# Optimization experiments

Measured on AMD Instinct MI355X. Metric: run time of the kernel, lower is better.

## Reference

```python
import jax, jax.numpy as jnp
import numpy as np

B = 8
A = 3
LEVEL_HW = [(200, 304), (100, 152), (50, 76), (25, 38), (13, 19)]
LEVEL_SIZES = [A * h * w for h, w in LEVEL_HW]  # anchors per level
N_TOTAL = sum(LEVEL_SIZES)                      # 242991
IMG_H, IMG_W = 800.0, 1216.0
PRE_NMS_TOP_N = 2000
POST_NMS_TOP_N = 100
NMS_THRESH = 0.7
MIN_SIZE = 1e-3
BBOX_XFORM_CLIP = float(np.log(1000.0 / 16.0))
NEG = -1e30


def setup_inputs() -> dict:
    key = jax.random.key(0)
    ks = jax.random.split(key, 2 * len(LEVEL_HW) + 3)
    inp = {}
    for i, (h, w) in enumerate(LEVEL_HW):
        inp[f"cls{i}"] = jax.random.normal(ks[2 * i], (B, A, h, w), dtype=jnp.float32)
        inp[f"box{i}"] = jax.random.normal(ks[2 * i + 1], (B, 4 * A, h, w), dtype=jnp.float32) * 0.5
    kc, kw, _ = ks[-3], ks[-2], ks[-1]
    c = jax.random.uniform(kc, (N_TOTAL, 2), dtype=jnp.float32) * jnp.array([IMG_W, IMG_H], jnp.float32)
    wh = 16.0 + jax.random.uniform(kw, (N_TOTAL, 2), dtype=jnp.float32) * 240.0
    inp["anchors"] = jnp.concatenate([c - 0.5 * wh, c + 0.5 * wh], axis=-1)  # x1y1x2y2
    return inp


def _permute_flatten(p, C):
    # [N, A*C, H, W] -> [N, H*W*A, C]  (matches permute_and_flatten)
    n, ac, h, w = p.shape
    a = ac // C
    return p.reshape(n, a, C, h, w).transpose(0, 3, 4, 1, 2).reshape(n, -1, C)


def _decode(deltas, anchors):
    wa = anchors[:, 2] - anchors[:, 0]
    ha = anchors[:, 3] - anchors[:, 1]
    cxa = anchors[:, 0] + 0.5 * wa
    cya = anchors[:, 1] + 0.5 * ha
    dx, dy = deltas[..., 0], deltas[..., 1]
    dw = jnp.minimum(deltas[..., 2], BBOX_XFORM_CLIP)
    dh = jnp.minimum(deltas[..., 3], BBOX_XFORM_CLIP)
    cx = dx * wa + cxa
    cy = dy * ha + cya
    pw = jnp.exp(dw) * wa
    ph = jnp.exp(dh) * ha
    return jnp.stack([cx - 0.5 * pw, cy - 0.5 * ph, cx + 0.5 * pw, cy + 0.5 * ph], axis=-1)


def _nms_single(boxes, scores, lvl, valid):
    # batched_nms: offset boxes by level so cross-level boxes never overlap
    off = lvl.astype(boxes.dtype)[:, None] * (max(IMG_H, IMG_W) + 1.0)
    b0 = boxes + off
    s0 = jnp.where(valid, scores, NEG)  # small-box removal -> impossible to pick
    order = jnp.argsort(-s0)
    b = b0[order]
    s = s0[order]
    areas = (b[:, 2] - b[:, 0]) * (b[:, 3] - b[:, 1])
    suppressed0 = s <= NEG / 2
    idx_range = jnp.arange(s.shape[0])

    def step(suppressed, _):
        avail = jnp.where(suppressed, NEG, s)
        i = jnp.argmax(avail)
        ok = avail[i] > NEG / 2
        bi = b[i]
        xx1 = jnp.maximum(b[:, 0], bi[0])
        yy1 = jnp.maximum(b[:, 1], bi[1])
        xx2 = jnp.minimum(b[:, 2], bi[2])
        yy2 = jnp.minimum(b[:, 3], bi[3])
        inter = jnp.maximum(xx2 - xx1, 0.0) * jnp.maximum(yy2 - yy1, 0.0)
        union = areas + areas[i] - inter
        iou = jnp.where(union > 0, inter / union, 0.0)
        sup_new = suppressed | (iou > NMS_THRESH) | (idx_range == i)
        return jnp.where(ok, sup_new, suppressed), (jnp.where(ok, order[i], 0), ok)

    _, (sel, selv) = jax.lax.scan(step, suppressed0, None, length=POST_NMS_TOP_N)
    out_boxes = jnp.where(selv[:, None], boxes[sel], 0.0)
    out_scores = jnp.where(selv, scores[sel], 0.0)
    return out_boxes, out_scores


def reference(cls0, cls1, cls2, cls3, cls4, box0, box1, box2, box3, box4, anchors):
    cls_levels = [cls0, cls1, cls2, cls3, cls4]
    box_levels = [box0, box1, box2, box3, box4]
    pred_class = jnp.concatenate([_permute_flatten(c, 1) for c in cls_levels], axis=1)  # [B,N,1]
    deltas = jnp.concatenate([_permute_flatten(b, 4) for b in box_levels], axis=1)      # [B,N,4]
    proposals = _decode(deltas, anchors)                                               # [B,N,4]
    scores = pred_class[..., 0]                                                        # [B,N]

    # per-level top-k; replicates the original's cumulative k = min(k, num_anchor)
    keep, lvl = [], []
    k, off = PRE_NMS_TOP_N, 0
    for li, n in enumerate(LEVEL_SIZES):
        k = min(k, n)
        _, idx = jax.lax.top_k(scores[:, off:off + n], k)
        keep.append(idx + off)
        lvl.append(jnp.full((k,), li, dtype=jnp.int32))
        off += n
    keep = jnp.concatenate(keep, axis=1)   # [B,K]
    lvl = jnp.concatenate(lvl)             # [K]

    prop = jnp.take_along_axis(proposals, keep[..., None], axis=1)  # [B,K,4]
    sc = jnp.take_along_axis(scores, keep, axis=1)                  # [B,K]
    prop = jnp.stack([
        jnp.clip(prop[..., 0], 0.0, IMG_W), jnp.clip(prop[..., 1], 0.0, IMG_H),
        jnp.clip(prop[..., 2], 0.0, IMG_W), jnp.clip(prop[..., 3], 0.0, IMG_H)], axis=-1)
    valid = ((prop[..., 2] - prop[..., 0]) >= MIN_SIZE) & ((prop[..., 3] - prop[..., 1]) >= MIN_SIZE)
    boxes_out, scores_out = jax.vmap(lambda bx, s, v: _nms_single(bx, s, lvl, v))(prop, sc, valid)
    return boxes_out, scores_out  # [B,100,4], [B,100]
```

## Files before the change

### kernel.cpp

```cpp
#include <hip/hip_runtime.h>
#include <cstdint>

#define NTOT 242991
#define BATCH 8
#define KTOT 8741
#define CAP 8192
#define NBIN 4096
#define CSTR 16
#define MEMTOT 1943928
#define SLICE 256
#define RSTR 9
#define BCAP 2048
#define NB2 2048
#define DBLK 9

__device__ __forceinline__ int level_of(int n) {
    if (n < 182400) return 0;
    if (n < 228000) return 1;
    if (n < 239400) return 2;
    if (n < 242250) return 3;
    return 4;
}

__device__ __forceinline__ void locate(int n, int& l, int& H, int& W, int& loc) {
    if (n < 182400)      { l = 0; H = 200; W = 304; loc = n; }
    else if (n < 228000) { l = 1; H = 100; W = 152; loc = n - 182400; }
    else if (n < 239400) { l = 2; H = 50;  W = 76;  loc = n - 228000; }
    else if (n < 242250) { l = 3; H = 25;  W = 38;  loc = n - 239400; }
    else                 { l = 4; H = 13;  W = 19;  loc = n - 242250; }
}

__device__ __forceinline__ int classify_bl(int x) {
    int l, HW;
    if (x < 1459200)      { l = 0; HW = 60800; }
    else if (x < 1824000) { l = 1; HW = 15200; x -= 1459200; }
    else if (x < 1915200) { l = 2; HW = 3800;  x -= 1824000; }
    else if (x < 1938000) { l = 3; HW = 950;   x -= 1915200; }
    else                  { l = 4; HW = 247;   x -= 1938000; }
    return (x / (3 * HW)) * 5 + l;
}

__device__ __forceinline__ void mem_decompose(int x, int& b, int& n, int& bl) {
    int HW, off, l;
    if (x < 1459200)      { l = 0; HW = 60800; off = 0; }
    else if (x < 1824000) { l = 1; HW = 15200; off = 182400; x -= 1459200; }
    else if (x < 1915200) { l = 2; HW = 3800;  off = 228000; x -= 1824000; }
    else if (x < 1938000) { l = 3; HW = 950;   off = 239400; x -= 1915200; }
    else                  { l = 4; HW = 247;   off = 242250; x -= 1938000; }
    int seg = 3 * HW;
    b = x / seg; int r = x - b * seg;
    int a = r / HW, pix = r - a * HW;
    n = off + pix * 3 + a;
    bl = b * 5 + l;
}

__device__ __forceinline__ float read_cls(int gid, const float* c0, const float* c1,
                                          const float* c2, const float* c3, const float* c4) {
    return (gid < 1459200) ? c0[gid] :
           (gid < 1824000) ? c1[gid - 1459200] :
           (gid < 1915200) ? c2[gid - 1824000] :
           (gid < 1938000) ? c3[gid - 1915200] : c4[gid - 1938000];
}

__device__ __forceinline__ uint32_t suffix_scan_1024(uint32_t g, uint32_t* lds16, int t) {
    int lane = t & 63, wid = t >> 6;
    uint32_t v = g;
#pragma unroll
    for (int o = 1; o < 64; o <<= 1) {
        uint32_t oth = __shfl_down(v, o, 64);
        if (lane + o < 64) v += oth;
    }
    if (lane == 0) lds16[wid] = v;
    __syncthreads();
    uint32_t w = 0;
    for (int q = wid + 1; q < 16; q++) w += lds16[q];
    __syncthreads();
    return v + w;
}

__device__ __forceinline__ uint32_t prefix_scan_1024(uint32_t g, uint32_t* lds16, int t) {
    int lane = t & 63, wid = t >> 6;
    uint32_t v = g;
#pragma unroll
    for (int o = 1; o < 64; o <<= 1) {
        uint32_t oth = __shfl_up(v, o, 64);
        if (lane >= o) v += oth;
    }
    if (lane == 63) lds16[wid] = v;
    __syncthreads();
    uint32_t w = 0;
    for (int q = 0; q < wid; q++) w += lds16[q];
    __syncthreads();
    return v + w;
}

__device__ __forceinline__ bool iou_hit(float bx1, float by1, float bx2, float by2, float ca,
                                        float4 sv) {
    float xx1 = fmaxf(bx1, sv.x), yy1 = fmaxf(by1, sv.y);
    float xx2 = fminf(bx2, sv.z), yy2 = fminf(by2, sv.w);
    float inter = fmaxf(xx2 - xx1, 0.f) * fmaxf(yy2 - yy1, 0.f);
    float sa = (sv.z - sv.x) * (sv.w - sv.y);
    float un = ca + sa - inter;
    return (un > 0.f) && (inter / un > 0.7f);
}

__global__ __launch_bounds__(1024)
void k_keys(const float* __restrict__ c0, const float* __restrict__ c1,
            const float* __restrict__ c2, const float* __restrict__ c3,
            const float* __restrict__ c4, uint32_t* __restrict__ hist) {
    int t = threadIdx.x;
    int base = blockIdx.x * 1024;
    int gid = base + t;
    bool in = gid < MEMTOT;
    __shared__ uint32_t lh[NBIN];

    int bl = 0, b, n;
    uint32_t u = 0;
    if (in) {
        mem_decompose(gid, b, n, bl);
        float sv = read_cls(gid, c0, c1, c2, c3, c4);
        u = __float_as_uint(sv);
        u ^= (u >> 31) ? 0xFFFFFFFFu : 0x80000000u;
    }
    int blf = classify_bl(base);
    int bll = classify_bl(min(base + 1023, MEMTOT - 1));
    if (blf == bll) {
        for (int j = t; j < NBIN; j += 1024) lh[j] = 0u;
        __syncthreads();
        if (in) atomicAdd(&lh[u >> 20], 1u);
        __syncthreads();
        uint32_t* gh = hist + (size_t)blf * NBIN;
        for (int j = t; j < NBIN; j += 1024) {
            uint32_t v = lh[j];
            if (v) atomicAdd(&gh[j], v);
        }
    } else {
        if (in) atomicAdd(&hist[(size_t)bl * NBIN + (u >> 20)], 1u);
    }
}

__global__ void k_bins(const uint32_t* __restrict__ hist, int* __restrict__ binT,
                       int* __restrict__ rrem) {
    int bl = blockIdx.x;
    const uint32_t* h = hist + (size_t)bl * NBIN;
    int l = bl % 5;
    uint32_t k = (l == 4) ? 741u : 2000u;
    __shared__ uint32_t ts[256];
    __shared__ uint32_t sb[256];
    int t = threadIdx.x;
    uint32_t hh[16];
#pragma unroll
    for (int i = 0; i < 16; i++) hh[i] = h[t * 16 + i];
    uint32_t s = 0;
#pragma unroll
    for (int i = 0; i < 16; i++) s += hh[i];
    ts[t] = s; sb[t] = s;
    __syncthreads();
    for (int d = 1; d < 256; d <<= 1) {
        uint32_t add = (t + d < 256) ? sb[t + d] : 0u;
        __syncthreads();
        sb[t] += add;
        __syncthreads();
    }
    uint32_t inc = sb[t], excl = inc - ts[t];
    if (excl < k && inc >= k) {
        uint32_t cum = excl;
#pragma unroll
        for (int i = 15; i >= 0; i--) {
            if (cum + hh[i] >= k) { binT[bl] = t * 16 + i; rrem[bl] = (int)(k - cum); break; }
            cum += hh[i];
        }
    }
}

__global__ __launch_bounds__(1024)
void k_compact(const float* __restrict__ c0, const float* __restrict__ c1,
               const float* __restrict__ c2, const float* __restrict__ c3,
               const float* __restrict__ c4, const int* __restrict__ binT,
               uint32_t* __restrict__ keep_n, uint32_t* __restrict__ keep_u,
               uint32_t* __restrict__ keep_cnt,
               uint32_t* __restrict__ cand_n, uint32_t* __restrict__ cand_u,
               uint32_t* __restrict__ cand_cnt) {
    int gid = blockIdx.x * 1024 + threadIdx.x;
    bool in = gid < MEMTOT;
    int b = 0, n = 0, bl = 0;
    uint32_t u = 0;
    if (in) {
        mem_decompose(gid, b, n, bl);
        float sv = read_cls(gid, c0, c1, c2, c3, c4);
        u = __float_as_uint(sv);
        u ^= (u >> 31) ? 0xFFFFFFFFu : 0x80000000u;
    }
    int T = in ? binT[bl] : 0x7FFFFFFF;
    int bin = (int)(u >> 20);
    bool pk = in && (bin > T);
    bool pc = in && (bin == T);
    int lane = threadIdx.x & 63;

    unsigned long long act = __ballot(in);
    if (act == 0ull) return;
    int lead = __ffsll(act) - 1;
    int bl0 = __shfl(bl, lead, 64);
    bool unif = (__ballot(in && (bl == bl0)) == act);
    if (unif) {
        int b0 = bl0 / 5, l0 = bl0 % 5;
        uint32_t kbase = (uint32_t)(b0 * KTOT + l0 * 2000);
        unsigned long long mk = __ballot(pk);
        if (mk) {
            int leader = __ffsll(mk) - 1;
            uint32_t bs = 0;
            if (lane == leader) bs = atomicAdd(&keep_cnt[bl0 * CSTR], (uint32_t)__popcll(mk));
            bs = __shfl(bs, leader, 64);
            if (pk) {
                uint32_t p = kbase + bs + (uint32_t)__popcll(mk & ((1ull << lane) - 1ull));
                keep_n[p] = (uint32_t)n; keep_u[p] = u;
            }
        }
        unsigned long long mc = __ballot(pc);
        if (mc) {
            int leader = __ffsll(mc) - 1;
            uint32_t bs = 0;
            if (lane == leader) bs = atomicAdd(&cand_cnt[bl0 * CSTR], (uint32_t)__popcll(mc));
            bs = __shfl(bs, leader, 64);
            if (pc) {
                uint32_t p = bs + (uint32_t)__popcll(mc & ((1ull << lane) - 1ull));
                if (p < CAP) {
                    cand_n[(size_t)bl0 * CAP + p] = (uint32_t)n;
                    cand_u[(size_t)bl0 * CAP + p] = u;
                }
            }
        }
    } else {
        int b1 = bl / 5, l1 = bl % 5;
        if (pk) {
            uint32_t p = atomicAdd(&keep_cnt[bl * CSTR], 1u);
            uint32_t q = (uint32_t)(b1 * KTOT + l1 * 2000) + p;
            keep_n[q] = (uint32_t)n; keep_u[q] = u;
        }
        if (pc) {
            uint32_t p = atomicAdd(&cand_cnt[bl * CSTR], 1u);
            if (p < CAP) {
                cand_n[(size_t)bl * CAP + p] = (uint32_t)n;
                cand_u[(size_t)bl * CAP + p] = u;
            }
        }
    }
}

__global__ __launch_bounds__(1024)
void k_select(const uint32_t* __restrict__ cand_n, const uint32_t* __restrict__ cand_u,
              const uint32_t* __restrict__ cand_cnt, const int* __restrict__ rrem,
              uint32_t* __restrict__ keep_n, uint32_t* __restrict__ keep_u,
              uint32_t* __restrict__ keep_cnt) {
    int bl = blockIdx.x;
    int b = bl / 5, l = bl % 5;
    int C = (int)min(cand_cnt[bl * CSTR], (uint32_t)CAP);
    int r = rrem[bl];
    const uint32_t* cdn = cand_n + (size_t)bl * CAP;
    const uint32_t* cdu = cand_u + (size_t)bl * CAP;
    __shared__ uint32_t hist_l[2048];
    __shared__ uint32_t lds16[16];
    __shared__ unsigned long long pref_sh;
    __shared__ uint32_t kk_sh;
    int t = threadIdx.x;
    if (t == 0) { pref_sh = 0ull; kk_sh = (uint32_t)r; }
    unsigned long long maskAcc = 0ull;
    const int shifts[5] = {41, 30, 19, 8, 0};
    const uint32_t masks[5] = {0x7FFu, 0x7FFu, 0x7FFu, 0x7FFu, 0xFFu};
    __syncthreads();
    for (int p = 0; p < 5; p++) {
        int shift = shifts[p];
        uint32_t msk = masks[p];
        for (int j = t; j < 2048; j += 1024) hist_l[j] = 0u;
        __syncthreads();
        unsigned long long pref = pref_sh;
        uint32_t kk = kk_sh;
        for (int i = t; i < C; i += 1024) {
            unsigned long long key =
                ((unsigned long long)cdu[i] << 32) | (uint32_t)(~cdn[i]);
            if ((key & maskAcc) == pref)
                atomicAdd(&hist_l[(uint32_t)(key >> shift) & msk], 1u);
        }
        __syncthreads();
        uint32_t g = hist_l[2 * t] + hist_l[2 * t + 1];
        uint32_t inc = suffix_scan_1024(g, lds16, t);
        uint32_t excl = inc - g;
        if (excl < kk && inc >= kk) {
            uint32_t hh1 = hist_l[2 * t + 1];
            uint32_t digit, rem;
            if (excl + hh1 >= kk) { digit = 2 * t + 1; rem = kk - excl; }
            else { digit = 2 * t; rem = kk - (excl + hh1); }
            pref_sh = pref | ((unsigned long long)digit << shift);
            kk_sh = rem;
        }
        __syncthreads();
        maskAcc |= (unsigned long long)msk << shift;
    }
    unsigned long long Tk = pref_sh;
    __syncthreads();
    int lane = t & 63;
    for (int i0 = 0; i0 < C; i0 += 1024) {
        int i = i0 + t;
        bool in = i < C;
        uint32_t n = in ? cdn[i] : 0u;
        uint32_t u = in ? cdu[i] : 0u;
        unsigned long long key = in ?
            (((unsigned long long)u << 32) | (uint32_t)(~n)) : 0ull;
        bool pr = in && ((key & maskAcc) >= Tk);
        unsigned long long mk = __ballot(pr);
        if (mk) {
            int leader = __ffsll(mk) - 1;
            uint32_t bs = 0;
            if (lane == leader) bs = atomicAdd(&keep_cnt[bl * CSTR], (uint32_t)__popcll(mk));
            bs = __shfl(bs, leader, 64);
            if (pr) {
                uint32_t p = (uint32_t)(b * KTOT + l * 2000) + bs +
                             (uint32_t)__popcll(mk & ((1ull << lane) - 1ull));
                keep_n[p] = n; keep_u[p] = u;
            }
        }
    }
}

__global__ __launch_bounds__(1024)
void k_decode(const float* __restrict__ b0, const float* __restrict__ b1,
              const float* __restrict__ b2, const float* __restrict__ b3,
              const float* __restrict__ b4, const float* __restrict__ anchors,
              const uint32_t* __restrict__ keep_n, const uint32_t* __restrict__ keep_u,
              float4* __restrict__ nbox, unsigned long long* __restrict__ nkey,
              uint32_t* __restrict__ shist) {
    int blk = blockIdx.x;
    int b = blk / DBLK, seg = blk % DBLK;
    int i = seg * 1024 + threadIdx.x;
    int t = threadIdx.x;
    __shared__ uint32_t lh[NBIN];
    for (int j = t; j < NBIN; j += 1024) lh[j] = 0u;
    __syncthreads();
    if (i < KTOT) {
        int gid = b * KTOT + i;
        int n = (int)keep_n[gid];
        uint32_t u = keep_u[gid];
        int l, H, W, loc; locate(n, l, H, W, loc);
        int a = loc % 3, hw = loc / 3;
        int w = hw % W, h = hw / W;
        const float* bp = (l == 0) ? b0 : (l == 1) ? b1 : (l == 2) ? b2 : (l == 3) ? b3 : b4;
        int HW = H * W;
        int base = ((b * 12 + a * 4) * H + h) * W + w;
        float dx = bp[base], dy = bp[base + HW];
        float dw = bp[base + 2 * HW], dh = bp[base + 3 * HW];
        float ax1 = anchors[4 * n], ay1 = anchors[4 * n + 1];
        float ax2 = anchors[4 * n + 2], ay2 = anchors[4 * n + 3];
        float wa = ax2 - ax1, ha = ay2 - ay1;
        float cxa = ax1 + 0.5f * wa, cya = ay1 + 0.5f * ha;
        const float CLIPV = 4.135166556742356f;
        dw = fminf(dw, CLIPV); dh = fminf(dh, CLIPV);
        float cx = dx * wa + cxa, cy = dy * ha + cya;
        float pw = expf(dw) * wa, ph = expf(dh) * ha;
        float x1 = cx - 0.5f * pw, y1 = cy - 0.5f * ph;
        float x2 = cx + 0.5f * pw, y2 = cy + 0.5f * ph;
        x1 = fminf(fmaxf(x1, 0.f), 1216.f); x2 = fminf(fmaxf(x2, 0.f), 1216.f);
        y1 = fminf(fmaxf(y1, 0.f), 800.f);  y2 = fminf(fmaxf(y2, 0.f), 800.f);
        bool valid = ((x2 - x1) >= 1e-3f) && ((y2 - y1) >= 1e-3f);
        float off = (float)l * 1217.0f;
        nbox[gid] = make_float4(x1 + off, y1 + off, x2 + off, y2 + off);
        nkey[gid] = valid ? (((unsigned long long)u << 32) | (uint32_t)(~n)) : 0ull;
        if (valid) atomicAdd(&lh[u >> 20], 1u);
    }
    __syncthreads();
    uint32_t* gh = shist + (size_t)b * NBIN;
    for (int j = t; j < NBIN; j += 1024) {
        uint32_t v = lh[j];
        if (v) atomicAdd(&gh[j], v);
    }
}

__global__ __launch_bounds__(1024)
void k_nms(const unsigned long long* __restrict__ nkey, const float4* __restrict__ nbox,
           const uint32_t* __restrict__ shist,
           unsigned long long* __restrict__ skey, float4* __restrict__ sbox,
           float* __restrict__ out) {
    int b = blockIdx.x, t = threadIdx.x, lane = t & 63, wid = t >> 6;
    unsigned long long* SK = skey + (size_t)b * KTOT;
    float4* BXs = sbox + (size_t)b * KTOT;

    __shared__ unsigned short bstart16[NBIN];
    __shared__ unsigned short bcnt16[NBIN];
    __shared__ unsigned long long k_l[BCAP];
    __shared__ unsigned short p_l[BCAP];
    __shared__ uint32_t scratch[4096];
    __shared__ float4 sel_l[100];
    __shared__ uint32_t sup[SLICE / 32];
    __shared__ uint32_t lds16[16];
    __shared__ uint32_t V_sh, picks_sh, bend_sh, fat_sh;
    __shared__ unsigned long long gmax_sh;
    __shared__ uint32_t jpos_sh;
    __shared__ unsigned long long wred[16];

    const uint32_t* H = shist + (size_t)b * NBIN;
    uint32_t h0 = H[4 * t], h1 = H[4 * t + 1], h2 = H[4 * t + 2], h3 = H[4 * t + 3];
    uint32_t g = h0 + h1 + h2 + h3;
    uint32_t inc = suffix_scan_1024(g, lds16, t);
    if (t == 0) { V_sh = inc; picks_sh = 0u; }
    uint32_t acc = inc - g;
    uint32_t* scur32 = scratch;
    bstart16[4 * t + 3] = (unsigned short)acc; bcnt16[4 * t + 3] = (unsigned short)h3;
    scur32[4 * t + 3] = acc; acc += h3;
    bstart16[4 * t + 2] = (unsigned short)acc; bcnt16[4 * t + 2] = (unsigned short)h2;
    scur32[4 * t + 2] = acc; acc += h2;
    bstart16[4 * t + 1] = (unsigned short)acc; bcnt16[4 * t + 1] = (unsigned short)h1;
    scur32[4 * t + 1] = acc; acc += h1;
    bstart16[4 * t + 0] = (unsigned short)acc; bcnt16[4 * t + 0] = (unsigned short)h0;
    scur32[4 * t + 0] = acc;
    __syncthreads();

#pragma unroll
    for (int e = 0; e < DBLK; e++) {
        int i = t + e * 1024;
        if (i < KTOT) {
            unsigned long long kk = nkey[(size_t)b * KTOT + i];
            if (kk != 0ull) {
                uint32_t q = (uint32_t)(kk >> 52);
                uint32_t p = atomicAdd(&scur32[q], 1u);
                SK[p] = kk;
                BXs[p] = nbox[(size_t)b * KTOT + i];
            }
        }
    }
    __threadfence();
    __syncthreads();

    uint32_t V = V_sh;
    uint32_t picks = 0;
    uint32_t P = 0;
    while (P < V && picks < 100u) {
        uint32_t target = min(P + (uint32_t)BCAP, V);
        if (t == 0) { bend_sh = P; fat_sh = P; }
        __syncthreads();
        for (int q = t; q < NBIN; q += 1024) {
            uint32_t c = bcnt16[q];
            if (c) {
                uint32_t s = bstart16[q];
                if (s >= P && s + c <= target) atomicMax(&bend_sh, s + c);
                if (s == P) fat_sh = P + c;
            }
        }
        __syncthreads();
        uint32_t B = bend_sh;

        if (B > P) {
            uint32_t total = B - P;
            uint32_t* hist2 = scratch;
            uint32_t* scur2 = scratch + 2048;
            for (int j = t; j < NB2; j += 1024) hist2[j] = 0u;
            __syncthreads();
            unsigned long long k0 = 0ull, k1 = 0ull;
            uint32_t bin0 = 0xFFFFFFFFu, bin1 = 0xFFFFFFFFu;
            uint32_t j0 = P + (uint32_t)t, j1 = P + (uint32_t)t + 1024u;
            if (j0 < B) {
                k0 = SK[j0];
                uint32_t q = (uint32_t)(k0 >> 52);
                uint32_t c = bcnt16[q], rel = (uint32_t)bstart16[q] - P;
                uint32_t sub = (uint32_t)((k0 >> 44) & 0xFFull);
                bin0 = rel + ((c * (255u - sub)) >> 8);
                atomicAdd(&hist2[bin0], 1u);
            }
            if (j1 < B) {
                k1 = SK[j1];
                uint32_t q = (uint32_t)(k1 >> 52);
                uint32_t c = bcnt16[q], rel = (uint32_t)bstart16[q] - P;
                uint32_t sub = (uint32_t)((k1 >> 44) & 0xFFull);
                bin1 = rel + ((c * (255u - sub)) >> 8);
                atomicAdd(&hist2[bin1], 1u);
            }
            __syncthreads();
            uint32_t g0 = hist2[2 * t], g1 = hist2[2 * t + 1];
            uint32_t incp = prefix_scan_1024(g0 + g1, lds16, t);
            uint32_t excl = incp - (g0 + g1);
            scur2[2 * t] = excl; scur2[2 * t + 1] = excl + g0;
            __syncthreads();
            if (bin0 != 0xFFFFFFFFu) {
                uint32_t pos = atomicAdd(&scur2[bin0], 1u);
                k_l[pos] = k0; p_l[pos] = (unsigned short)j0;
            }
            if (bin1 != 0xFFFFFFFFu) {
                uint32_t pos = atomicAdd(&scur2[bin1], 1u);
                k_l[pos] = k1; p_l[pos] = (unsigned short)j1;
            }
            __syncthreads();
#pragma unroll
            for (int qq = 0; qq < 2; qq++) {
                uint32_t bin = 2 * (uint32_t)t + (uint32_t)qq;
                uint32_t c = hist2[bin];
                if (c > 1u) {
                    uint32_t st = scur2[bin] - c;
                    for (uint32_t a = st + 1; a < st + c; a++) {
                        unsigned long long kv = k_l[a]; unsigned short pv = p_l[a];
                        uint32_t w2 = a;
                        while (w2 > st && k_l[w2 - 1] < kv) {
                            k_l[w2] = k_l[w2 - 1]; p_l[w2] = p_l[w2 - 1]; w2--;
                        }
                        k_l[w2] = kv; p_l[w2] = pv;
                    }
                }
            }
            __syncthreads();

            float* box_x = (float*)scratch;
            float* box_y = box_x + SLICE;
            float* box_z = box_y + SLICE;
            float* box_w = box_z + SLICE;
            uint32_t* rows = scratch + 1024;
            for (uint32_t s0 = 0; s0 < total && picks < 100u; s0 += SLICE) {
                uint32_t sl = min((uint32_t)SLICE, total - s0);
                __syncthreads();
                if (t < SLICE) {
                    if (t < (int)sl) {
                        float4 cb = BXs[p_l[s0 + t]];
                        box_x[t] = cb.x; box_y[t] = cb.y; box_z[t] = cb.z; box_w[t] = cb.w;
                    } else {
                        box_x[t] = 0.f; box_y[t] = 0.f; box_z[t] = 0.f; box_w[t] = 0.f;
                    }
                }
                if (t < SLICE / 32) sup[t] = 0u;
                __syncthreads();
                if (picks > 0u && t < (int)sl) {
                    float bx1 = box_x[t], by1 = box_y[t], bx2 = box_z[t], by2 = box_w[t];
                    float ca = (bx2 - bx1) * (by2 - by1);
                    bool hit = false;
                    uint32_t s = 0;
                    for (; s + 4 <= picks; s += 4) {
                        float4 v0 = sel_l[s], v1 = sel_l[s + 1], v2 = sel_l[s + 2],
                               v3 = sel_l[s + 3];
                        hit = hit | iou_hit(bx1, by1, bx2, by2, ca, v0)
                                  | iou_hit(bx1, by1, bx2, by2, ca, v1)
                                  | iou_hit(bx1, by1, bx2, by2, ca, v2)
                                  | iou_hit(bx1, by1, bx2, by2, ca, v3);
                    }
                    for (; s < picks; s++) hit = hit | iou_hit(bx1, by1, bx2, by2, ca, sel_l[s]);
                    if (hit) atomicOr(&sup[t >> 5], 1u << (t & 31));
                }
                for (uint32_t widx = t; widx < SLICE * 8; widx += 1024) {
                    uint32_t i = widx & (SLICE - 1);
                    uint32_t wq = widx >> 8;
                    float bx1 = box_x[i], by1 = box_y[i], bx2 = box_z[i], by2 = box_w[i];
                    float ai = (bx2 - bx1) * (by2 - by1);
                    uint32_t jbase = wq * 32u, bits = 0u;
#pragma unroll
                    for (uint32_t qq = 0; qq < 32u; qq++) {
                        uint32_t jj = jbase + qq;
                        float jx1 = box_x[jj], jy1 = box_y[jj],
                              jx2 = box_z[jj], jy2 = box_w[jj];
                        float xx1 = fmaxf(bx1, jx1), yy1 = fmaxf(by1, jy1);
                        float xx2 = fminf(bx2, jx2), yy2 = fminf(by2, jy2);
                        float inter = fmaxf(xx2 - xx1, 0.f) * fmaxf(yy2 - yy1, 0.f);
                        float aj = (jx2 - jx1) * (jy2 - jy1);
                        float un = ai + aj - inter;
                        bool sp = (jj > i) && (un > 0.f) && (inter / un > 0.7f);
                        bits |= ((uint32_t)sp) << qq;
                    }
                    rows[i * RSTR + wq] = bits;
                }
                __syncthreads();
                if (wid == 0) {
                    uint32_t myw = (lane < SLICE / 32) ? sup[lane] : 0u;
                    uint32_t pk = picks;
                    for (uint32_t i = 0; i < sl && pk < 100u; i++) {
                        uint32_t wv = __shfl(myw, (int)(i >> 5), 64);
                        if (!((wv >> (i & 31)) & 1u)) {
                            if (lane < SLICE / 32) myw |= rows[i * RSTR + lane];
                            if (lane == 0) {
                                float4 cb = make_float4(box_x[i], box_y[i], box_z[i], box_w[i]);
                                sel_l[pk] = cb;
                                unsigned long long mkey = k_l[s0 + i];
                                uint32_t n = ~(uint32_t)(mkey & 0xFFFFFFFFull);
                                float off = (float)level_of((int)n) * 1217.0f;
                                float* ob = out + ((size_t)b * 100 + pk) * 4;
                                ob[0] = cb.x - off; ob[1] = cb.y - off;
                                ob[2] = cb.z - off; ob[3] = cb.w - off;
                                uint32_t uu = (uint32_t)(mkey >> 32);
                                uint32_t sb2 = (uu & 0x80000000u) ? (uu ^ 0x80000000u) : ~uu;
                                out[3200 + b * 100 + pk] = __uint_as_float(sb2);
                            }
                            pk++;
                        }
                    }
                    if (lane == 0) picks_sh = pk;
                }
                __syncthreads();
                picks = picks_sh;
            }
            __syncthreads();
        } else {
            B = fat_sh;
            uint32_t cnt = B - P;
            unsigned long long last = 0ull;
            bool first = true;
            for (uint32_t done = 0; done < cnt && picks < 100u; done++) {
                unsigned long long lbest = 0ull;
                uint32_t jbest = 0;
                for (uint32_t jj = P + t; jj < B; jj += 1024) {
                    unsigned long long kk = SK[jj];
                    if ((first || kk < last) && kk > lbest) { lbest = kk; jbest = jj; }
                }
                unsigned long long wm = lbest;
#pragma unroll
                for (int o2 = 32; o2 > 0; o2 >>= 1) {
                    unsigned long long oth = __shfl_down(wm, o2, 64);
                    if (oth > wm) wm = oth;
                }
                if (lane == 0) wred[wid] = wm;
                __syncthreads();
                if (t == 0) {
                    unsigned long long mm = wred[0];
                    for (int q = 1; q < 16; q++) if (wred[q] > mm) mm = wred[q];
                    gmax_sh = mm;
                }
                __syncthreads();
                unsigned long long gm = gmax_sh;
                if (gm == 0ull) break;
                if (lbest == gm) jpos_sh = jbest;
                __syncthreads();
                float4 cb = BXs[jpos_sh];
                float ca = (cb.z - cb.x) * (cb.w - cb.y);
                bool hit = false;
                for (uint32_t s = (uint32_t)lane; s < picks; s += 64u)
                    hit = hit | iou_hit(cb.x, cb.y, cb.z, cb.w, ca, sel_l[s]);
                bool selq = (__ballot(hit) == 0ull);
                if (selq) {
                    if (t == 0) {
                        sel_l[picks] = cb;
                        uint32_t n = ~(uint32_t)(gm & 0xFFFFFFFFull);
                        float off = (float)level_of((int)n) * 1217.0f;
                        float* ob = out + ((size_t)b * 100 + picks) * 4;
                        ob[0] = cb.x - off; ob[1] = cb.y - off;
                        ob[2] = cb.z - off; ob[3] = cb.w - off;
                        uint32_t uu = (uint32_t)(gm >> 32);
                        uint32_t sb2 = (uu & 0x80000000u) ? (uu ^ 0x80000000u) : ~uu;
                        out[3200 + b * 100 + picks] = __uint_as_float(sb2);
                    }
                    picks++;
                }
                last = gm; first = false;
                __syncthreads();
            }
        }
        P = B;
        __syncthreads();
    }
    for (uint32_t i = picks + (uint32_t)t; i < 100u; i += 1024u) {
        float* ob = out + ((size_t)b * 100 + i) * 4;
        ob[0] = 0.f; ob[1] = 0.f; ob[2] = 0.f; ob[3] = 0.f;
        out[3200 + b * 100 + i] = 0.f;
    }
}

extern "C" void kernel_launch(void* const* d_in, const int* in_sizes, int n_in,
                              void* d_out, int out_size, void* d_ws, size_t ws_size,
                              hipStream_t stream) {
    const float* cls[5] = { (const float*)d_in[0], (const float*)d_in[2], (const float*)d_in[4],
                            (const float*)d_in[6], (const float*)d_in[8] };
    const float* box[5] = { (const float*)d_in[1], (const float*)d_in[3], (const float*)d_in[5],
                            (const float*)d_in[7], (const float*)d_in[9] };
    const float* anchors = (const float*)d_in[10];
    float* out = (float*)d_out;

    uint32_t* W32 = (uint32_t*)d_ws;
    size_t o = 0;
    uint32_t* hist     = W32 + o; o += (size_t)40 * NBIN;
    uint32_t* shist    = W32 + o; o += (size_t)BATCH * NBIN;
    uint32_t* keep_cnt = W32 + o; o += 40 * CSTR;
    uint32_t* cand_cnt = W32 + o; o += 40 * CSTR;
    size_t zero_n = o;
    int*      binT     = (int*)(W32 + o); o += 64;
    int*      rrem     = (int*)(W32 + o); o += 64;
    uint32_t* keep_n   = W32 + o; o += (size_t)BATCH * KTOT;
    uint32_t* keep_u   = W32 + o; o += (size_t)BATCH * KTOT;
    uint32_t* cand_n   = W32 + o; o += (size_t)40 * CAP;
    uint32_t* cand_u   = W32 + o; o += (size_t)40 * CAP;
    o = (o + 3) & ~(size_t)3;
    float4* nbox = (float4*)(W32 + o); o += (size_t)BATCH * KTOT * 4;
    unsigned long long* nkey = (unsigned long long*)(W32 + o); o += (size_t)BATCH * KTOT * 2;
    float4* sbox = (float4*)(W32 + o); o += (size_t)BATCH * KTOT * 4;
    unsigned long long* skey = (unsigned long long*)(W32 + o); o += (size_t)BATCH * KTOT * 2;

    hipMemsetAsync(d_ws, 0, zero_n * sizeof(uint32_t), stream);
    k_keys<<<(MEMTOT + 1023) / 1024, 1024, 0, stream>>>(cls[0], cls[1], cls[2], cls[3], cls[4],
                                                        hist);
    k_bins<<<40, 256, 0, stream>>>(hist, binT, rrem);
    k_compact<<<(MEMTOT + 1023) / 1024, 1024, 0, stream>>>(cls[0], cls[1], cls[2], cls[3],
                                                           cls[4], binT, keep_n, keep_u,
                                                           keep_cnt, cand_n, cand_u, cand_cnt);
    k_select<<<40, 1024, 0, stream>>>(cand_n, cand_u, cand_cnt, rrem, keep_n, keep_u, keep_cnt);
    k_decode<<<BATCH * DBLK, 1024, 0, stream>>>(box[0], box[1], box[2], box[3], box[4],
                                                anchors, keep_n, keep_u, nbox, nkey, shist);
    k_nms<<<BATCH, 1024, 0, stream>>>(nkey, nbox, shist, skey, sbox, out);
}
```

Before: 147.8 us.

## Drop global bin-scatter of keys/boxes in NMS; filter unsorted keys per batch window

The NMS kernel no longer scatters all per-image keys and boxes into bucket-sorted global arrays up front. Each window iteration instead rescans the full unsorted key array and keeps only keys whose coarse bin falls in the current window. The fat-bin fallback also scans everything, and the window-end reduction now uses a wave shuffle max before the atomic. This removes a global write/read pass and a threadfence, but each window and each fat-bin pick now re-reads all 8741 keys.

```diff
diff --git a/kernel.cpp b/kernel.cpp
--- a/kernel.cpp
+++ b/kernel.cpp
@@ -376,12 +376,10 @@
 
 __global__ __launch_bounds__(1024)
 void k_nms(const unsigned long long* __restrict__ nkey, const float4* __restrict__ nbox,
-           const uint32_t* __restrict__ shist,
-           unsigned long long* __restrict__ skey, float4* __restrict__ sbox,
-           float* __restrict__ out) {
+           const uint32_t* __restrict__ shist, float* __restrict__ out) {
     int b = blockIdx.x, t = threadIdx.x, lane = t & 63, wid = t >> 6;
-    unsigned long long* SK = skey + (size_t)b * KTOT;
-    float4* BXs = sbox + (size_t)b * KTOT;
+    const unsigned long long* NK = nkey + (size_t)b * KTOT;
+    const float4* NB = nbox + (size_t)b * KTOT;
 
     __shared__ unsigned short bstart16[NBIN];
     __shared__ unsigned short bcnt16[NBIN];
@@ -402,31 +400,10 @@
     uint32_t inc = suffix_scan_1024(g, lds16, t);
     if (t == 0) { V_sh = inc; picks_sh = 0u; }
     uint32_t acc = inc - g;
-    uint32_t* scur32 = scratch;
-    bstart16[4 * t + 3] = (unsigned short)acc; bcnt16[4 * t + 3] = (unsigned short)h3;
-    scur32[4 * t + 3] = acc; acc += h3;
-    bstart16[4 * t + 2] = (unsigned short)acc; bcnt16[4 * t + 2] = (unsigned short)h2;
-    scur32[4 * t + 2] = acc; acc += h2;
-    bstart16[4 * t + 1] = (unsigned short)acc; bcnt16[4 * t + 1] = (unsigned short)h1;
-    scur32[4 * t + 1] = acc; acc += h1;
+    bstart16[4 * t + 3] = (unsigned short)acc; bcnt16[4 * t + 3] = (unsigned short)h3; acc += h3;
+    bstart16[4 * t + 2] = (unsigned short)acc; bcnt16[4 * t + 2] = (unsigned short)h2; acc += h2;
+    bstart16[4 * t + 1] = (unsigned short)acc; bcnt16[4 * t + 1] = (unsigned short)h1; acc += h1;
     bstart16[4 * t + 0] = (unsigned short)acc; bcnt16[4 * t + 0] = (unsigned short)h0;
-    scur32[4 * t + 0] = acc;
-    __syncthreads();
-
-#pragma unroll
-    for (int e = 0; e < DBLK; e++) {
-        int i = t + e * 1024;
-        if (i < KTOT) {
-            unsigned long long kk = nkey[(size_t)b * KTOT + i];
-            if (kk != 0ull) {
-                uint32_t q = (uint32_t)(kk >> 52);
-                uint32_t p = atomicAdd(&scur32[q], 1u);
-                SK[p] = kk;
-                BXs[p] = nbox[(size_t)b * KTOT + i];
-            }
-        }
-    }
-    __threadfence();
     __syncthreads();
 
     uint32_t V = V_sh;
@@ -436,13 +413,22 @@
         uint32_t target = min(P + (uint32_t)BCAP, V);
         if (t == 0) { bend_sh = P; fat_sh = P; }
         __syncthreads();
-        for (int q = t; q < NBIN; q += 1024) {
-            uint32_t c = bcnt16[q];
-            if (c) {
-                uint32_t s = bstart16[q];
-                if (s >= P && s + c <= target) atomicMax(&bend_sh, s + c);
-                if (s == P) fat_sh = P + c;
-            }
+        {
+            uint32_t lmax = P;
+            for (int q = t; q < NBIN; q += 1024) {
+                uint32_t c = bcnt16[q];
+                if (c) {
+                    uint32_t s = bstart16[q];
+                    if (s >= P && s + c <= target) lmax = max(lmax, s + c);
+                    if (s == P) fat_sh = P + c;
+                }
+            }
+#pragma unroll
+            for (int o = 32; o > 0; o >>= 1) {
+                uint32_t oth = __shfl_down(lmax, o, 64);
+                lmax = max(lmax, oth);
+            }
+            if (lane == 0) atomicMax(&bend_sh, lmax);
         }
         __syncthreads();
         uint32_t B = bend_sh;
@@ -453,24 +439,22 @@
             uint32_t* scur2 = scratch + 2048;
             for (int j = t; j < NB2; j += 1024) hist2[j] = 0u;
             __syncthreads();
-            unsigned long long k0 = 0ull, k1 = 0ull;
-            uint32_t bin0 = 0xFFFFFFFFu, bin1 = 0xFFFFFFFFu;
-            uint32_t j0 = P + (uint32_t)t, j1 = P + (uint32_t)t + 1024u;
-            if (j0 < B) {
-                k0 = SK[j0];
-                uint32_t q = (uint32_t)(k0 >> 52);
-                uint32_t c = bcnt16[q], rel = (uint32_t)bstart16[q] - P;
-                uint32_t sub = (uint32_t)((k0 >> 44) & 0xFFull);
-                bin0 = rel + ((c * (255u - sub)) >> 8);
-                atomicAdd(&hist2[bin0], 1u);
-            }
-            if (j1 < B) {
-                k1 = SK[j1];
-                uint32_t q = (uint32_t)(k1 >> 52);
-                uint32_t c = bcnt16[q], rel = (uint32_t)bstart16[q] - P;
-                uint32_t sub = (uint32_t)((k1 >> 44) & 0xFFull);
-                bin1 = rel + ((c * (255u - sub)) >> 8);
-                atomicAdd(&hist2[bin1], 1u);
+#pragma unroll
+            for (int e = 0; e < DBLK; e++) {
+                int i = t + e * 1024;
+                if (i < KTOT) {
+                    unsigned long long kk = NK[i];
+                    if (kk != 0ull) {
+                        uint32_t q = (uint32_t)(kk >> 52);
+                        uint32_t s = bstart16[q];
+                        if (s >= P && s < B) {
+                            uint32_t c = bcnt16[q];
+                            uint32_t sub = (uint32_t)((kk >> 44) & 0xFFull);
+                            uint32_t bin = (s - P) + ((c * (255u - sub)) >> 8);
+                            atomicAdd(&hist2[bin], 1u);
+                        }
+                    }
+                }
             }
             __syncthreads();
             uint32_t g0 = hist2[2 * t], g1 = hist2[2 * t + 1];
@@ -478,13 +462,23 @@
             uint32_t excl = incp - (g0 + g1);
             scur2[2 * t] = excl; scur2[2 * t + 1] = excl + g0;
             __syncthreads();
-            if (bin0 != 0xFFFFFFFFu) {
-                uint32_t pos = atomicAdd(&scur2[bin0], 1u);
-                k_l[pos] = k0; p_l[pos] = (unsigned short)j0;
-            }
-            if (bin1 != 0xFFFFFFFFu) {
-                uint32_t pos = atomicAdd(&scur2[bin1], 1u);
-                k_l[pos] = k1; p_l[pos] = (unsigned short)j1;
+#pragma unroll
+            for (int e = 0; e < DBLK; e++) {
+                int i = t + e * 1024;
+                if (i < KTOT) {
+                    unsigned long long kk = NK[i];
+                    if (kk != 0ull) {
+                        uint32_t q = (uint32_t)(kk >> 52);
+                        uint32_t s = bstart16[q];
+                        if (s >= P && s < B) {
+                            uint32_t c = bcnt16[q];
+                            uint32_t sub = (uint32_t)((kk >> 44) & 0xFFull);
+                            uint32_t bin = (s - P) + ((c * (255u - sub)) >> 8);
+                            uint32_t pos = atomicAdd(&scur2[bin], 1u);
+                            k_l[pos] = kk; p_l[pos] = (unsigned short)i;
+                        }
+                    }
+                }
             }
             __syncthreads();
 #pragma unroll
@@ -515,7 +509,7 @@
                 __syncthreads();
                 if (t < SLICE) {
                     if (t < (int)sl) {
-                        float4 cb = BXs[p_l[s0 + t]];
+                        float4 cb = NB[p_l[s0 + t]];
                         box_x[t] = cb.x; box_y[t] = cb.y; box_z[t] = cb.z; box_w[t] = cb.w;
                     } else {
                         box_x[t] = 0.f; box_y[t] = 0.f; box_z[t] = 0.f; box_w[t] = 0.f;
@@ -593,14 +587,16 @@
         } else {
             B = fat_sh;
             uint32_t cnt = B - P;
+            unsigned short Pw = (unsigned short)P;
             unsigned long long last = 0ull;
             bool first = true;
             for (uint32_t done = 0; done < cnt && picks < 100u; done++) {
                 unsigned long long lbest = 0ull;
                 uint32_t jbest = 0;
-                for (uint32_t jj = P + t; jj < B; jj += 1024) {
-                    unsigned long long kk = SK[jj];
-                    if ((first || kk < last) && kk > lbest) { lbest = kk; jbest = jj; }
+                for (uint32_t jj = t; jj < KTOT; jj += 1024) {
+                    unsigned long long kk = NK[jj];
+                    if (kk != 0ull && bstart16[(uint32_t)(kk >> 52)] == Pw &&
+                        (first || kk < last) && kk > lbest) { lbest = kk; jbest = jj; }
                 }
                 unsigned long long wm = lbest;
 #pragma unroll
@@ -620,7 +616,7 @@
                 if (gm == 0ull) break;
                 if (lbest == gm) jpos_sh = jbest;
                 __syncthreads();
-                float4 cb = BXs[jpos_sh];
+                float4 cb = NB[jpos_sh];
                 float ca = (cb.z - cb.x) * (cb.w - cb.y);
                 bool hit = false;
                 for (uint32_t s = (uint32_t)lane; s < picks; s += 64u)
@@ -680,8 +676,6 @@
     o = (o + 3) & ~(size_t)3;
     float4* nbox = (float4*)(W32 + o); o += (size_t)BATCH * KTOT * 4;
     unsigned long long* nkey = (unsigned long long*)(W32 + o); o += (size_t)BATCH * KTOT * 2;
-    float4* sbox = (float4*)(W32 + o); o += (size_t)BATCH * KTOT * 4;
-    unsigned long long* skey = (unsigned long long*)(W32 + o); o += (size_t)BATCH * KTOT * 2;
 
     hipMemsetAsync(d_ws, 0, zero_n * sizeof(uint32_t), stream);
     k_keys<<<(MEMTOT + 1023) / 1024, 1024, 0, stream>>>(cls[0], cls[1], cls[2], cls[3], cls[4],
@@ -693,5 +687,5 @@
     k_select<<<40, 1024, 0, stream>>>(cand_n, cand_u, cand_cnt, rrem, keep_n, keep_u, keep_cnt);
     k_decode<<<BATCH * DBLK, 1024, 0, stream>>>(box[0], box[1], box[2], box[3], box[4],
                                                 anchors, keep_n, keep_u, nbox, nkey, shist);
-    k_nms<<<BATCH, 1024, 0, stream>>>(nkey, nbox, shist, skey, sbox, out);
-}
+    k_nms<<<BATCH, 1024, 0, stream>>>(nkey, nbox, shist, out);
+}
```

New measurement: 136.3 us (median of 2 runs). 1.08x faster.
